# Kernel tuning notes

Measured on AMD Instinct MI355X. Metric: run time of the kernel, lower is better.

## Reference

```python
import jax, jax.numpy as jnp
import numpy as np

N, E, D_IN, D_OUT, H = 50000, 800000, 128, 128, 4
D_H = D_OUT // H


def setup_inputs() -> dict:
    key = jax.random.key(0)
    ks = jax.random.split(key, 6)
    x = jax.random.normal(ks[0], (N, D_IN), dtype=jnp.float32)
    edge_index = jax.random.randint(ks[1], (2, E), 0, N, dtype=jnp.int64)
    # parameters (xavier-ish scaling)
    W = jax.random.normal(ks[2], (D_IN, D_OUT), dtype=jnp.float32) * (1.0 / np.sqrt(D_IN))
    attn_vec = jax.random.normal(ks[3], (H, 2 * D_H), dtype=jnp.float32) * (1.0 / np.sqrt(2 * D_H))
    out_w = jax.random.normal(ks[4], (D_OUT, D_OUT), dtype=jnp.float32) * (1.0 / np.sqrt(D_OUT))
    out_b = jax.random.normal(ks[5], (D_OUT,), dtype=jnp.float32) * 0.01
    return {"x": x, "edge_index": edge_index, "W": W, "attn_vec": attn_vec,
            "out_w": out_w, "out_b": out_b}


def reference(x, edge_index, W, attn_vec, out_w, out_b):
    n = x.shape[0]
    Wx = (x @ W).reshape(n, H, D_H)                      # [N,H,d_h]
    src, dst = edge_index[0], edge_index[1]
    h_src = Wx[src]                                      # [E,H,d_h]
    h_dst = Wx[dst]                                      # [E,H,d_h]
    a_i = attn_vec[:, :D_H]                              # [H,d_h]
    a_j = attn_vec[:, D_H:]                              # [H,d_h]
    e = jnp.einsum('ehd,hd->eh', h_src, a_i) + jnp.einsum('ehd,hd->eh', h_dst, a_j)
    e = jax.nn.leaky_relu(e, negative_slope=0.2)         # [E,H]
    # segment softmax over incoming edges per destination node
    e_max = jax.ops.segment_max(e, dst, num_segments=n)  # [N,H]
    exp_e = jnp.exp(e - e_max[dst])                      # [E,H]
    exp_sum = jax.ops.segment_sum(exp_e, dst, num_segments=n)  # [N,H]
    alpha = exp_e / (exp_sum[dst] + 1e-16)               # [E,H]
    # weighted scatter-add aggregation
    agg = jax.ops.segment_sum(alpha[:, :, None] * h_src, dst, num_segments=n)  # [N,H,d_h]
    out = agg.reshape(n, D_OUT) @ out_w + out_b
    return jax.nn.elu(out)
```

## Files before the change

### kernel.cpp

```cpp
#include <hip/hip_runtime.h>
#include <math.h>


typedef __attribute__((ext_vector_type(8))) short short8;
typedef __attribute__((ext_vector_type(4))) float f32x4;

#define BIN_VPT 16

__device__ __forceinline__ float lrelu(float v) { return v >= 0.f ? v : 0.2f * v; }

__device__ __forceinline__ unsigned short f2bf(float f) {
  unsigned int u = __float_as_uint(f);
  u += 0x7FFFu + ((u >> 16) & 1u);
  return (unsigned short)(u >> 16);
}
__device__ __forceinline__ unsigned int cvt_pk_bf16(float lo, float hi) {
  unsigned int r;
  asm("v_cvt_pk_bf16_f32 %0, %1, %2" : "=v"(r) : "v"(lo), "v"(hi));
  return r;
}
__device__ __forceinline__ float bflo(unsigned int w) { return __uint_as_float(w << 16); }
__device__ __forceinline__ float bfhi(unsigned int w) { return __uint_as_float(w & 0xFFFF0000u); }

__device__ __forceinline__ int blk_excl_scan(int v, int* ws) {
  const int t = threadIdx.x, lane = t & 63, wv = t >> 6;
  int incl = v;
#pragma unroll
  for (int m = 1; m < 64; m <<= 1) {
    int x = __shfl_up(incl, m, 64);
    if (lane >= m) incl += x;
  }
  if (lane == 63) ws[wv] = incl;
  __syncthreads();
  int woff = 0;
  for (int p = 0; p < wv; ++p) woff += ws[p];
  return woff + incl - v;
}

__global__ void k_setup(const float* __restrict__ W, const float* __restrict__ ow,
                        unsigned short* __restrict__ wf, unsigned short* __restrict__ owf,
                        int* __restrict__ gcnt, int* __restrict__ gcur) {
  const int t = blockIdx.x * 256 + threadIdx.x;
  if (blockIdx.x == 0) gcnt[threadIdx.x] = 0;
  if (blockIdx.x == 1) gcur[threadIdx.x] = 0;
  const int which = t >> 11;
  const int tt = t & 2047;
  const float* M = which ? ow : W;
  unsigned short* F = which ? owf : wf;
  const int lane = tt & 63;
  const int nt = (tt >> 6) & 7;
  const int ks = tt >> 9;
  const int k0 = ks * 32 + (lane >> 4) * 8;
  const int col = nt * 16 + (lane & 15);
  short8 v;
#pragma unroll
  for (int j = 0; j < 8; ++j) v[j] = (short)f2bf(M[(k0 + j) * 128 + col]);
  *(short8*)(F + (size_t)tt * 8) = v;
}

__global__ void k_gemm1b(const float* __restrict__ x, const unsigned short* __restrict__ wf,
                         const float* __restrict__ attn, unsigned int* __restrict__ Wxb,
                         float* __restrict__ s_i, float* __restrict__ s_j, int n,
                         const int* __restrict__ dst, int* __restrict__ gcnt, int E,
                         int gemmBlocks) {
  __shared__ int lc[256];
  if (blockIdx.x >= gemmBlocks) {
    const int bb = blockIdx.x - gemmBlocks;
    lc[threadIdx.x] = 0;
    __syncthreads();
    const int base = bb * (256 * BIN_VPT);
#pragma unroll
    for (int j = 0; j < BIN_VPT; ++j) {
      int e = base + j * 256 + threadIdx.x;
      if (e < E) atomicAdd(&lc[((unsigned int)dst[e]) >> 8], 1);
    }
    __syncthreads();
    int c = lc[threadIdx.x];
    if (c) atomicAdd(&gcnt[threadIdx.x], c);
    return;
  }

  const int lane = threadIdx.x & 63;
  const int gw = blockIdx.x * (blockDim.x >> 6) + (threadIdx.x >> 6);
  const int r0 = gw * 16;
  if (r0 >= n) return;
  const int g = lane >> 4, c = lane & 15;

  f32x4 acc[8];
#pragma unroll
  for (int nt = 0; nt < 8; ++nt) acc[nt] = (f32x4){0.f, 0.f, 0.f, 0.f};

  const int arow = min(r0 + c, n - 1);
#pragma unroll
  for (int ks = 0; ks < 4; ++ks) {
    const float* xr = x + (size_t)arow * 128 + ks * 32 + g * 8;
    float4 v0 = *(const float4*)xr;
    float4 v1 = *(const float4*)(xr + 4);
    uint4 au;
    au.x = cvt_pk_bf16(v0.x, v0.y);
    au.y = cvt_pk_bf16(v0.z, v0.w);
    au.z = cvt_pk_bf16(v1.x, v1.y);
    au.w = cvt_pk_bf16(v1.z, v1.w);
    short8 af = __builtin_bit_cast(short8, au);
#pragma unroll
    for (int nt = 0; nt < 8; ++nt) {
      short8 bf = *(const short8*)(wf + ((size_t)(ks * 8 + nt) * 64 + lane) * 8);
      acc[nt] = __builtin_amdgcn_mfma_f32_16x16x32_bf16(af, bf, acc[nt], 0, 0, 0);
    }
  }

  const int odd = c & 1;
#pragma unroll
  for (int r = 0; r < 4; ++r) {
    const int row = r0 + g * 4 + r;
    if (row >= n) continue;
    unsigned int* dp = Wxb + (size_t)row * 64;
#pragma unroll
    for (int ntp = 0; ntp < 4; ++ntp) {
      float ve = acc[ntp][r], vo = acc[ntp + 4][r];
      float vex = __shfl_xor(ve, 1, 64);
      float vox = __shfl_xor(vo, 1, 64);
      const int nt = odd ? ntp + 4 : ntp;
      dp[nt * 8 + (c >> 1)] = cvt_pk_bf16(odd ? vox : ve, odd ? vo : vex);
    }
  }

  float aiv[8], ajv[8];
#pragma unroll
  for (int nt = 0; nt < 8; ++nt) {
    const int hh = nt >> 1, ch = (nt & 1) * 16 + c;
    aiv[nt] = attn[hh * 64 + ch];
    ajv[nt] = attn[hh * 64 + 32 + ch];
  }
#pragma unroll
  for (int r = 0; r < 4; ++r) {
    float pih[4], pjh[4];
#pragma unroll
    for (int h = 0; h < 4; ++h) {
      pih[h] = acc[2 * h][r] * aiv[2 * h] + acc[2 * h + 1][r] * aiv[2 * h + 1];
      pjh[h] = acc[2 * h][r] * ajv[2 * h] + acc[2 * h + 1][r] * ajv[2 * h + 1];
    }
#pragma unroll
    for (int m = 1; m < 16; m <<= 1) {
#pragma unroll
      for (int h = 0; h < 4; ++h) {
        pih[h] += __shfl_xor(pih[h], m, 64);
        pjh[h] += __shfl_xor(pjh[h], m, 64);
      }
    }
    const int row = r0 + g * 4 + r;
    if (c == 0 && row < n) {
#pragma unroll
      for (int h = 0; h < 4; ++h) {
        s_i[(size_t)row * 4 + h] = pih[h];
        s_j[(size_t)row * 4 + h] = pjh[h];
      }
    }
  }
}

__global__ void k_bin1(const int* __restrict__ edges, const int* __restrict__ gcnt,
                       int* __restrict__ gcur, unsigned int* __restrict__ tmp, int E) {
  __shared__ int ws[4];
  __shared__ int bst_s[256];
  __shared__ int lcnt[256];
  __shared__ int lbase[256];
  const int t = threadIdx.x;
  const int excl = blk_excl_scan(gcnt[t], ws);
  bst_s[t] = excl;
  lcnt[t] = 0;
  __syncthreads();
  const int base = blockIdx.x * (256 * BIN_VPT);
  unsigned int pv[BIN_VPT];
  int rk[BIN_VPT];
#pragma unroll
  for (int j = 0; j < BIN_VPT; ++j) {
    int e = base + j * 256 + t;
    if (e < E) {
      unsigned int s = (unsigned int)edges[e];
      unsigned int d = (unsigned int)edges[E + e];
      pv[j] = s | (d << 16);
      rk[j] = atomicAdd(&lcnt[d >> 8], 1);
    } else {
      pv[j] = 0u;
      rk[j] = -1;
    }
  }
  __syncthreads();
  const int c = lcnt[t];
  lbase[t] = bst_s[t] + (c ? atomicAdd(&gcur[t], c) : 0);
  __syncthreads();
#pragma unroll
  for (int j = 0; j < BIN_VPT; ++j) {
    if (rk[j] >= 0) {
      const int b = pv[j] >> 24;
      tmp[lbase[b] + rk[j]] = pv[j];
    }
  }
}

__global__ void k_bin2(const unsigned int* __restrict__ tmp, const int* __restrict__ gcnt,
                       int* __restrict__ csr, int* __restrict__ offs,
                       int* __restrict__ cnts, int n) {
  __shared__ int ws[4];
  __shared__ int bst_s[256];
  __shared__ int nc[256];
  const int b = blockIdx.x;
  const int t = threadIdx.x;
  bst_s[t] = blk_excl_scan(gcnt[t], ws);
  nc[t] = 0;
  __syncthreads();
  const int base = bst_s[b], cnt = gcnt[b];
  for (int i = t; i < cnt; i += 256)
    atomicAdd(&nc[(tmp[base + i] >> 16) & 255], 1);
  __syncthreads();
  const int node = b * 256 + t;
  const int c = nc[t];
  if (node < n) cnts[node] = c;
  __syncthreads();
  const int excl = blk_excl_scan(c, ws);
  if (node < n) offs[node] = base + excl;
  __syncthreads();
  nc[t] = excl;
  __syncthreads();
  for (int i = t; i < cnt; i += 256) {
    unsigned int v = tmp[base + i];
    int pos = atomicAdd(&nc[(v >> 16) & 255], 1);
    csr[base + pos] = (int)(v & 0xFFFFu);
  }
}

__global__ void k_aggm(const unsigned int* __restrict__ Wxb, const float* __restrict__ s_i,
                       const float* __restrict__ s_j, const int* __restrict__ offs,
                       const int* __restrict__ cnts, const int* __restrict__ csr_src,
                       const unsigned short* __restrict__ owf, const float* __restrict__ ob,
                       float* __restrict__ out, int n) {
  __shared__ unsigned int aTile[16][65];
  __shared__ int   lsrc[16][64];
  __shared__ float lp[16][64][4];
  const int lane = threadIdx.x & 63;
  const int wv = threadIdx.x >> 6;
  const int nd0 = blockIdx.x * 16;
  const int nd = nd0 + wv;
  const int h = lane >> 4;

  int base = 0, deg = 0;
  float4 sj = make_float4(0.f, 0.f, 0.f, 0.f);
  if (nd < n) {
    base = offs[nd];
    deg = cnts[nd];
    sj = *(const float4*)(s_j + (size_t)nd * 4);
  }

  float4 smp = make_float4(0.f, 0.f, 0.f, 0.f);
  float2 acc = make_float2(0.f, 0.f);
  for (int c0 = 0; c0 < deg; c0 += 64) {
    const int m = min(64, deg - c0);
    if (lane < m) {
      int src = csr_src[base + c0 + lane];
      float4 si = *(const float4*)(s_i + (size_t)src * 4);
      float4 p;
      p.x = __expf(lrelu(si.x + sj.x));
      p.y = __expf(lrelu(si.y + sj.y));
      p.z = __expf(lrelu(si.z + sj.z));
      p.w = __expf(lrelu(si.w + sj.w));
      smp.x += p.x; smp.y += p.y; smp.z += p.z; smp.w += p.w;
      lsrc[wv][lane] = src;
      *(float4*)&lp[wv][lane][0] = p;
    }
    asm volatile("s_waitcnt lgkmcnt(0)" ::: "memory");
    int k = 0;
    for (; k + 8 <= m; k += 8) {
      int s0 = lsrc[wv][k + 0], s1 = lsrc[wv][k + 1];
      int s2 = lsrc[wv][k + 2], s3 = lsrc[wv][k + 3];
      int s4 = lsrc[wv][k + 4], s5 = lsrc[wv][k + 5];
      int s6 = lsrc[wv][k + 6], s7 = lsrc[wv][k + 7];
      float p0 = lp[wv][k + 0][h], p1 = lp[wv][k + 1][h];
      float p2 = lp[wv][k + 2][h], p3 = lp[wv][k + 3][h];
      float p4 = lp[wv][k + 4][h], p5 = lp[wv][k + 5][h];
      float p6 = lp[wv][k + 6][h], p7 = lp[wv][k + 7][h];
      unsigned int w0 = Wxb[(size_t)s0 * 64 + lane];
      unsigned int w1 = Wxb[(size_t)s1 * 64 + lane];
      unsigned int w2 = Wxb[(size_t)s2 * 64 + lane];
      unsigned int w3 = Wxb[(size_t)s3 * 64 + lane];
      unsigned int w4 = Wxb[(size_t)s4 * 64 + lane];
      unsigned int w5 = Wxb[(size_t)s5 * 64 + lane];
      unsigned int w6 = Wxb[(size_t)s6 * 64 + lane];
      unsigned int w7 = Wxb[(size_t)s7 * 64 + lane];
      acc.x += p0 * bflo(w0); acc.y += p0 * bfhi(w0);
      acc.x += p1 * bflo(w1); acc.y += p1 * bfhi(w1);
      acc.x += p2 * bflo(w2); acc.y += p2 * bfhi(w2);
      acc.x += p3 * bflo(w3); acc.y += p3 * bfhi(w3);
      acc.x += p4 * bflo(w4); acc.y += p4 * bfhi(w4);
      acc.x += p5 * bflo(w5); acc.y += p5 * bfhi(w5);
      acc.x += p6 * bflo(w6); acc.y += p6 * bfhi(w6);
      acc.x += p7 * bflo(w7); acc.y += p7 * bfhi(w7);
    }
    for (; k + 4 <= m; k += 4) {
      int s0 = lsrc[wv][k + 0], s1 = lsrc[wv][k + 1];
      int s2 = lsrc[wv][k + 2], s3 = lsrc[wv][k + 3];
      float p0 = lp[wv][k + 0][h], p1 = lp[wv][k + 1][h];
      float p2 = lp[wv][k + 2][h], p3 = lp[wv][k + 3][h];
      unsigned int w0 = Wxb[(size_t)s0 * 64 + lane];
      unsigned int w1 = Wxb[(size_t)s1 * 64 + lane];
      unsigned int w2 = Wxb[(size_t)s2 * 64 + lane];
      unsigned int w3 = Wxb[(size_t)s3 * 64 + lane];
      acc.x += p0 * bflo(w0); acc.y += p0 * bfhi(w0);
      acc.x += p1 * bflo(w1); acc.y += p1 * bfhi(w1);
      acc.x += p2 * bflo(w2); acc.y += p2 * bfhi(w2);
      acc.x += p3 * bflo(w3); acc.y += p3 * bfhi(w3);
    }
    for (; k < m; ++k) {
      int s = lsrc[wv][k];
      float pv = lp[wv][k][h];
      unsigned int w = Wxb[(size_t)s * 64 + lane];
      acc.x += pv * bflo(w); acc.y += pv * bfhi(w);
    }
  }
#pragma unroll
  for (int m = 1; m < 64; m <<= 1) {
    smp.x += __shfl_xor(smp.x, m, 64);
    smp.y += __shfl_xor(smp.y, m, 64);
    smp.z += __shfl_xor(smp.z, m, 64);
    smp.w += __shfl_xor(smp.w, m, 64);
  }
  float sh = (h & 2) ? ((h & 1) ? smp.w : smp.z) : ((h & 1) ? smp.y : smp.x);
  const float inv = 1.f / (sh + 1e-16f);
  aTile[wv][lane] = cvt_pk_bf16(acc.x * inv, acc.y * inv);
  __syncthreads();

  if (wv < 8) {
    const int g = lane >> 4, c = lane & 15;
    const int nt = wv;
    f32x4 o = (f32x4){0.f, 0.f, 0.f, 0.f};
#pragma unroll
    for (int ks = 0; ks < 4; ++ks) {
      uint4 au = *(const uint4*)&aTile[c][ks * 16 + g * 4];
      short8 af = __builtin_bit_cast(short8, au);
      short8 bf = *(const short8*)(owf + ((size_t)(ks * 8 + nt) * 64 + lane) * 8);
      o = __builtin_amdgcn_mfma_f32_16x16x32_bf16(af, bf, o, 0, 0, 0);
    }
#pragma unroll
    for (int r = 0; r < 4; ++r) {
      const int row = nd0 + g * 4 + r;
      if (row < n) {
        float v = o[r] + ob[nt * 16 + c];
        v = v > 0.f ? v : expm1f(v);
        out[(size_t)row * 128 + nt * 16 + c] = v;
      }
    }
  }
}

extern "C" void kernel_launch(void* const* d_in, const int* in_sizes, int n_in,
                              void* d_out, int out_size, void* d_ws, size_t ws_size,
                              hipStream_t stream) {
  const float* x    = (const float*)d_in[0];
  const int*   edges = (const int*)d_in[1];
  const float* W    = (const float*)d_in[2];
  const float* attn = (const float*)d_in[3];
  const float* ow   = (const float*)d_in[4];
  const float* ob   = (const float*)d_in[5];
  const int n = in_sizes[0] / 128;
  const int E = in_sizes[1] / 2;
  float* out = (float*)d_out;

  char* wp = (char*)d_ws;
  auto alloc = [&](size_t bytes) {
    char* p = wp;
    wp += (bytes + 255) & ~(size_t)255;
    return p;
  };
  unsigned short* wf  = (unsigned short*)alloc(2048 * 8 * 2);
  unsigned short* owf = (unsigned short*)alloc(2048 * 8 * 2);
  unsigned int*   Wxb = (unsigned int*)alloc((size_t)n * 64 * 4);
  float* s_i    = (float*)alloc((size_t)n * 4 * 4);
  float* s_j    = (float*)alloc((size_t)n * 4 * 4);
  int*   gcnt   = (int*)alloc(256 * 4);
  int*   gcur   = (int*)alloc(256 * 4);
  int*   offs   = (int*)alloc((size_t)n * 4);
  int*   cnts   = (int*)alloc((size_t)n * 4);
  unsigned int* tmp = (unsigned int*)alloc((size_t)E * 4);
  int*   csr    = (int*)alloc((size_t)E * 4);

  dim3 blk(256);
  const int NB = (n + 255) / 256;
  const int EB = (E + 256 * BIN_VPT - 1) / (256 * BIN_VPT);
  const int strips = (n + 15) / 16;
  const int gemmBlocks = (strips + 3) / 4;

  k_setup<<<16, blk, 0, stream>>>(W, ow, wf, owf, gcnt, gcur);
  k_gemm1b<<<gemmBlocks + EB, blk, 0, stream>>>(x, wf, attn, Wxb, s_i, s_j, n,
                                                edges + E, gcnt, E, gemmBlocks);
  k_bin1<<<EB, blk, 0, stream>>>(edges, gcnt, gcur, tmp, E);
  k_bin2<<<NB, blk, 0, stream>>>(tmp, gcnt, csr, offs, cnts, n);
  k_aggm<<<(n + 15) / 16, dim3(1024), 0, stream>>>(Wxb, s_i, s_j, offs, cnts, csr,
                                                   owf, ob, out, n);
}
```

Baseline: 104.1 us.

## Process four destination nodes per wavefront in aggregation kernel

The aggregation kernel now assigns four consecutive destination nodes to each wavefront and uses 256-thread blocks instead of 1024. Their CSR edge lists are walked as one contiguous stream, so a wave fills up to 64 edge lanes across node boundaries rather than leaving lanes idle on low-degree nodes. Softmax denominators are summed per node inside the edge loop, and each wave runs two output MFMA tiles. This cuts per-wave setup and the underused-lane waste seen at average degree around 16, but adds serial per-node bookkeeping and lowers parallelism per block.

```diff
diff --git a/kernel.cpp b/kernel.cpp
--- a/kernel.cpp
+++ b/kernel.cpp
@@ -230,108 +230,98 @@
   }
 }
 
+#define AGG_EDGE(e)                                                     \
+  {                                                                     \
+    int s_ = lsrc[wv][e];                                               \
+    float p_ = lp[wv][e][h];                                            \
+    unsigned int w_ = Wxb[(unsigned)(s_ << 6) | (unsigned)lane];        \
+    acc.x += p_ * bflo(w_);                                             \
+    acc.y += p_ * bfhi(w_);                                             \
+    smh += p_;                                                          \
+  }
+
 __global__ void k_aggm(const unsigned int* __restrict__ Wxb, const float* __restrict__ s_i,
                        const float* __restrict__ s_j, const int* __restrict__ offs,
                        const int* __restrict__ cnts, const int* __restrict__ csr_src,
                        const unsigned short* __restrict__ owf, const float* __restrict__ ob,
                        float* __restrict__ out, int n) {
   __shared__ unsigned int aTile[16][65];
-  __shared__ int   lsrc[16][64];
-  __shared__ float lp[16][64][4];
+  __shared__ int   lsrc[4][64];
+  __shared__ float lp[4][64][4];
   const int lane = threadIdx.x & 63;
   const int wv = threadIdx.x >> 6;
   const int nd0 = blockIdx.x * 16;
-  const int nd = nd0 + wv;
+  const int nd0w = nd0 + wv * 4;
   const int h = lane >> 4;
 
-  int base = 0, deg = 0;
-  float4 sj = make_float4(0.f, 0.f, 0.f, 0.f);
-  if (nd < n) {
-    base = offs[nd];
-    deg = cnts[nd];
-    sj = *(const float4*)(s_j + (size_t)nd * 4);
-  }
-
-  float4 smp = make_float4(0.f, 0.f, 0.f, 0.f);
+  int degv = 0;
+  if (lane < 4 && nd0w + lane < n) degv = cnts[nd0w + lane];
+  const int wbase = (nd0w < n) ? offs[nd0w] : 0;
+  const int d0 = __shfl(degv, 0, 64), d1 = __shfl(degv, 1, 64);
+  const int d2 = __shfl(degv, 2, 64), d3 = __shfl(degv, 3, 64);
+  const int b0 = d0, b1 = d0 + d1, b2 = b1 + d2;
+  const int tot = b2 + d3;
+
+  int cur = 0;
+  int rem = d0;
   float2 acc = make_float2(0.f, 0.f);
-  for (int c0 = 0; c0 < deg; c0 += 64) {
-    const int m = min(64, deg - c0);
+  float smh = 0.f;
+
+  while (cur < 4 && rem == 0) {
+    if (nd0w + cur < n) aTile[(wv << 2) + cur][lane] = 0u;
+    ++cur;
+    rem = (cur == 1) ? d1 : (cur == 2) ? d2 : (cur == 3) ? d3 : 0;
+  }
+
+  for (int c0 = 0; c0 < tot; c0 += 64) {
+    const int m = min(64, tot - c0);
     if (lane < m) {
-      int src = csr_src[base + c0 + lane];
-      float4 si = *(const float4*)(s_i + (size_t)src * 4);
+      const int pos = c0 + lane;
+      const int src = csr_src[wbase + pos];
+      const int nl = (pos >= b0) + (pos >= b1) + (pos >= b2);
+      const float4 sj = *(const float4*)(s_j + (size_t)(nd0w + nl) * 4);
+      const float4 si = *(const float4*)(s_i + (size_t)src * 4);
       float4 p;
       p.x = __expf(lrelu(si.x + sj.x));
       p.y = __expf(lrelu(si.y + sj.y));
       p.z = __expf(lrelu(si.z + sj.z));
       p.w = __expf(lrelu(si.w + sj.w));
-      smp.x += p.x; smp.y += p.y; smp.z += p.z; smp.w += p.w;
       lsrc[wv][lane] = src;
       *(float4*)&lp[wv][lane][0] = p;
     }
     asm volatile("s_waitcnt lgkmcnt(0)" ::: "memory");
     int k = 0;
-    for (; k + 8 <= m; k += 8) {
-      int s0 = lsrc[wv][k + 0], s1 = lsrc[wv][k + 1];
-      int s2 = lsrc[wv][k + 2], s3 = lsrc[wv][k + 3];
-      int s4 = lsrc[wv][k + 4], s5 = lsrc[wv][k + 5];
-      int s6 = lsrc[wv][k + 6], s7 = lsrc[wv][k + 7];
-      float p0 = lp[wv][k + 0][h], p1 = lp[wv][k + 1][h];
-      float p2 = lp[wv][k + 2][h], p3 = lp[wv][k + 3][h];
-      float p4 = lp[wv][k + 4][h], p5 = lp[wv][k + 5][h];
-      float p6 = lp[wv][k + 6][h], p7 = lp[wv][k + 7][h];
-      unsigned int w0 = Wxb[(size_t)s0 * 64 + lane];
-      unsigned int w1 = Wxb[(size_t)s1 * 64 + lane];
-      unsigned int w2 = Wxb[(size_t)s2 * 64 + lane];
-      unsigned int w3 = Wxb[(size_t)s3 * 64 + lane];
-      unsigned int w4 = Wxb[(size_t)s4 * 64 + lane];
-      unsigned int w5 = Wxb[(size_t)s5 * 64 + lane];
-      unsigned int w6 = Wxb[(size_t)s6 * 64 + lane];
-      unsigned int w7 = Wxb[(size_t)s7 * 64 + lane];
-      acc.x += p0 * bflo(w0); acc.y += p0 * bfhi(w0);
-      acc.x += p1 * bflo(w1); acc.y += p1 * bfhi(w1);
-      acc.x += p2 * bflo(w2); acc.y += p2 * bfhi(w2);
-      acc.x += p3 * bflo(w3); acc.y += p3 * bfhi(w3);
-      acc.x += p4 * bflo(w4); acc.y += p4 * bfhi(w4);
-      acc.x += p5 * bflo(w5); acc.y += p5 * bfhi(w5);
-      acc.x += p6 * bflo(w6); acc.y += p6 * bfhi(w6);
-      acc.x += p7 * bflo(w7); acc.y += p7 * bfhi(w7);
-    }
-    for (; k + 4 <= m; k += 4) {
-      int s0 = lsrc[wv][k + 0], s1 = lsrc[wv][k + 1];
-      int s2 = lsrc[wv][k + 2], s3 = lsrc[wv][k + 3];
-      float p0 = lp[wv][k + 0][h], p1 = lp[wv][k + 1][h];
-      float p2 = lp[wv][k + 2][h], p3 = lp[wv][k + 3][h];
-      unsigned int w0 = Wxb[(size_t)s0 * 64 + lane];
-      unsigned int w1 = Wxb[(size_t)s1 * 64 + lane];
-      unsigned int w2 = Wxb[(size_t)s2 * 64 + lane];
-      unsigned int w3 = Wxb[(size_t)s3 * 64 + lane];
-      acc.x += p0 * bflo(w0); acc.y += p0 * bfhi(w0);
-      acc.x += p1 * bflo(w1); acc.y += p1 * bfhi(w1);
-      acc.x += p2 * bflo(w2); acc.y += p2 * bfhi(w2);
-      acc.x += p3 * bflo(w3); acc.y += p3 * bfhi(w3);
-    }
-    for (; k < m; ++k) {
-      int s = lsrc[wv][k];
-      float pv = lp[wv][k][h];
-      unsigned int w = Wxb[(size_t)s * 64 + lane];
-      acc.x += pv * bflo(w); acc.y += pv * bfhi(w);
-    }
-  }
-#pragma unroll
-  for (int m = 1; m < 64; m <<= 1) {
-    smp.x += __shfl_xor(smp.x, m, 64);
-    smp.y += __shfl_xor(smp.y, m, 64);
-    smp.z += __shfl_xor(smp.z, m, 64);
-    smp.w += __shfl_xor(smp.w, m, 64);
-  }
-  float sh = (h & 2) ? ((h & 1) ? smp.w : smp.z) : ((h & 1) ? smp.y : smp.x);
-  const float inv = 1.f / (sh + 1e-16f);
-  aTile[wv][lane] = cvt_pk_bf16(acc.x * inv, acc.y * inv);
-  __syncthreads();
-
-  if (wv < 8) {
-    const int g = lane >> 4, c = lane & 15;
-    const int nt = wv;
+    while (k < m) {
+      const int take = min(m - k, rem);
+      int e = k;
+      const int end = k + take;
+      for (; e + 8 <= end; e += 8) {
+        AGG_EDGE(e + 0) AGG_EDGE(e + 1) AGG_EDGE(e + 2) AGG_EDGE(e + 3)
+        AGG_EDGE(e + 4) AGG_EDGE(e + 5) AGG_EDGE(e + 6) AGG_EDGE(e + 7)
+      }
+      for (; e + 4 <= end; e += 4) {
+        AGG_EDGE(e + 0) AGG_EDGE(e + 1) AGG_EDGE(e + 2) AGG_EDGE(e + 3)
+      }
+      for (; e < end; ++e) AGG_EDGE(e)
+      k += take;
+      rem -= take;
+      while (rem == 0 && cur < 4) {
+        const float inv = 1.f / (smh + 1e-16f);
+        if (nd0w + cur < n)
+          aTile[(wv << 2) + cur][lane] = cvt_pk_bf16(acc.x * inv, acc.y * inv);
+        ++cur;
+        acc.x = 0.f; acc.y = 0.f; smh = 0.f;
+        rem = (cur == 1) ? d1 : (cur == 2) ? d2 : (cur == 3) ? d3 : 0;
+      }
+      if (cur >= 4) break;
+    }
+  }
+  __syncthreads();
+
+  const int g = lane >> 4, c = lane & 15;
+#pragma unroll
+  for (int t2 = 0; t2 < 2; ++t2) {
+    const int nt = wv + t2 * 4;
     f32x4 o = (f32x4){0.f, 0.f, 0.f, 0.f};
 #pragma unroll
     for (int ks = 0; ks < 4; ++ks) {
@@ -394,6 +384,6 @@
                                                 edges + E, gcnt, E, gemmBlocks);
   k_bin1<<<EB, blk, 0, stream>>>(edges, gcnt, gcur, tmp, E);
   k_bin2<<<NB, blk, 0, stream>>>(tmp, gcnt, csr, offs, cnts, n);
-  k_aggm<<<(n + 15) / 16, dim3(1024), 0, stream>>>(Wxb, s_i, s_j, offs, cnts, csr,
-                                                   owf, ob, out, n);
-}
+  k_aggm<<<(n + 15) / 16, blk, 0, stream>>>(Wxb, s_i, s_j, offs, cnts, csr,
+                                            owf, ob, out, n);
+}
```

New measurement: 96.16 us. 1.08x faster.
